# Optimization experiments

Measured on AMD Instinct MI355X. Metric: run time of the kernel, lower is better.

## Reference

```python
import jax, jax.numpy as jnp
import numpy as np

B, S, D = 4, 2048, 1024
E, TOP_K = 8, 2
N_FF = 4096
H = int(2 * N_FF / 3)  # 2730, Expert hidden when ffn_multiplier is None


def setup_inputs() -> dict:
    key = jax.random.key(0)
    ks = jax.random.split(key, 8)
    s = 0.02
    return {
        "x": jax.random.normal(ks[0], (B, S, D), jnp.float32),
        "noise": jax.random.normal(ks[1], (B, S, E), jnp.float32),
        "w_route": jax.random.normal(ks[2], (D, E), jnp.float32) * s,
        "b_route": jnp.zeros((E,), jnp.float32),
        "w_noise": jax.random.normal(ks[3], (D, E), jnp.float32) * s,
        "b_noise": jnp.zeros((E,), jnp.float32),
        "w_proj": jax.random.normal(ks[4], (E, D, 2 * H), jnp.float32) * s,  # SwiGLU proj per expert
        "w_down": jax.random.normal(ks[5], (E, H, D), jnp.float32) * s,
    }


def reference(x, noise, w_route, b_route, w_noise, b_noise, w_proj, w_down):
    b, s, d = x.shape
    e = w_route.shape[1]
    n = b * s
    capacity = int(n * TOP_K / e * 1.0)  # capacity_factor = 1.0

    # --- NoisyTopkRouter (temperature = 1.0) ---
    logits = jnp.einsum("bsd,de->bse", x, w_route) + b_route
    noise_scale = jax.nn.softplus(jnp.einsum("bsd,de->bse", x, w_noise) + b_noise)
    noisy = logits + noise * noise_scale
    top_v, top_i = jax.lax.top_k(noisy, TOP_K)  # [b,s,k]
    # softmax over -inf-filled sparse logits == softmax over the top-k values,
    # scattered back to the expert axis
    probs_k = jax.nn.softmax(top_v, axis=-1)  # [b,s,k]
    routing = jnp.sum(jax.nn.one_hot(top_i, e, dtype=x.dtype) * probs_k[..., None], axis=-2)  # [b,s,e]
    router_prob = routing.mean(axis=(0, 1))
    aux_loss = jnp.sum((router_prob - 1.0 / e) ** 2)

    # --- dispatch ---
    flat_x = x.reshape(n, d)
    flat_gate = routing.reshape(n, e)
    hit = jnp.any(top_i.reshape(n, TOP_K)[:, :, None] == jnp.arange(e)[None, None, :], axis=1)  # [n,e]

    def per_expert(mask_e, gate_e, wp, wd):
        # keep first `capacity` selected tokens, in token order (matches torch nonzero order)
        keep = mask_e & (jnp.cumsum(mask_e) <= capacity)
        sel = jnp.argsort(~keep, stable=True)[:capacity]  # selected token ids first, in order
        valid = keep[sel].astype(flat_x.dtype)
        xin = flat_x[sel]  # [capacity, d]
        x1, x2 = jnp.split(xin @ wp, 2, axis=-1)
        out = (jax.nn.silu(x1) * x2) @ wd  # [capacity, d]
        w = gate_e[sel] * valid
        return sel, out * w[:, None]

    sel, contrib = jax.vmap(per_expert)(hit.T, flat_gate.T, w_proj, w_down)  # [e,cap], [e,cap,d]
    updates = jnp.zeros_like(flat_x).at[sel.reshape(-1)].add(contrib.reshape(-1, d))
    return updates.reshape(b, s, d), aux_loss
```

## Files before the change

kernel.cpp:

```cpp
#include <hip/hip_runtime.h>
#include <cstdint>
#include <cstddef>

#define NTOK 8192
#define DMODEL 1024
#define NEXP 8
#define CAP 2048
#define HFF 2730
#define HFF2 5460
#define KPAD 2752

typedef float f32x4 __attribute__((ext_vector_type(4)));
typedef __attribute__((ext_vector_type(8))) short short8;

__device__ inline unsigned short f2bf(float f) {
  union { float f; unsigned u; } v; v.f = f;
  unsigned u = v.u;
  return (unsigned short)((u + 0x7FFFu + ((u >> 16) & 1u)) >> 16);
}
__device__ inline float bf2f(unsigned short s) {
  union { unsigned u; float f; } v; v.u = ((unsigned)s) << 16; return v.f;
}

typedef __attribute__((address_space(1))) const void g_void;
typedef __attribute__((address_space(3))) void l_void;
__device__ __forceinline__ void dma16(const void* g, void* l) {
  __builtin_amdgcn_global_load_lds((g_void*)g, (l_void*)l, 16, 0, 0);
}
__device__ __forceinline__ void keep(short8 v) { asm volatile("" :: "v"(v)); }

__global__ void cast_x_kernel(const float* __restrict__ x, unsigned short* __restrict__ xb) {
  size_t i = ((size_t)blockIdx.x * 256 + threadIdx.x) * 8;
  float4 v0 = *(const float4*)(x + i);
  float4 v1 = *(const float4*)(x + i + 4);
  union { short8 v; unsigned short s[8]; } p;
  p.s[0] = f2bf(v0.x); p.s[1] = f2bf(v0.y); p.s[2] = f2bf(v0.z); p.s[3] = f2bf(v0.w);
  p.s[4] = f2bf(v1.x); p.s[5] = f2bf(v1.y); p.s[6] = f2bf(v1.z); p.s[7] = f2bf(v1.w);
  *(short8*)(xb + i) = p.v;
}

__global__ void router_kernel(const float* __restrict__ x,
                              const float* __restrict__ noise,
                              const float* __restrict__ w_route,
                              const float* __restrict__ b_route,
                              const float* __restrict__ w_noise,
                              const float* __restrict__ b_noise,
                              int* __restrict__ topi,
                              float* __restrict__ gates) {
  const int lane = threadIdx.x & 63;
  const int wave = threadIdx.x >> 6;
  const int tok = blockIdx.x * 4 + wave;
  const float* xr = x + (size_t)tok * DMODEL;

  double aR[8], aN[8];
#pragma unroll
  for (int e = 0; e < 8; e++) { aR[e] = 0.0; aN[e] = 0.0; }

  for (int d = lane; d < DMODEL; d += 64) {
    double xv = (double)xr[d];
    const float* wr = w_route + d * 8;
    const float* wn = w_noise + d * 8;
#pragma unroll
    for (int e = 0; e < 8; e++) {
      aR[e] += xv * (double)wr[e];
      aN[e] += xv * (double)wn[e];
    }
  }
#pragma unroll
  for (int off = 32; off > 0; off >>= 1) {
#pragma unroll
    for (int e = 0; e < 8; e++) {
      aR[e] += __shfl_down(aR[e], (unsigned)off, 64);
      aN[e] += __shfl_down(aN[e], (unsigned)off, 64);
    }
  }
  if (lane == 0) {
    double nv[8];
#pragma unroll
    for (int e = 0; e < 8; e++) {
      double lg = aR[e] + (double)b_route[e];
      double ns = aN[e] + (double)b_noise[e];
      double sp = fmax(ns, 0.0) + log1p(exp(-fabs(ns)));
      nv[e] = lg + (double)noise[(size_t)tok * 8 + e] * sp;
    }
    int i0 = 0;
#pragma unroll
    for (int e = 1; e < 8; e++) if (nv[e] > nv[i0]) i0 = e;
    int i1 = (i0 == 0) ? 1 : 0;
#pragma unroll
    for (int e = 0; e < 8; e++) if (e != i0 && nv[e] > nv[i1]) i1 = e;
    double r = exp(nv[i1] - nv[i0]);
    float g0 = (float)(1.0 / (1.0 + r));
    float g1 = (float)(r / (1.0 + r));
    topi[tok * 2] = i0; topi[tok * 2 + 1] = i1;
    gates[tok * 2] = g0; gates[tok * 2 + 1] = g1;
  }
}

__global__ void aux_kernel(const int* __restrict__ topi,
                           const float* __restrict__ gates,
                           float* __restrict__ out) {
  const int t = threadIdx.x;
  float s[8];
#pragma unroll
  for (int e = 0; e < 8; e++) s[e] = 0.f;
  for (int i = t; i < NTOK; i += 256) {
    int i0 = topi[2 * i], i1 = topi[2 * i + 1];
    float g0 = gates[2 * i], g1 = gates[2 * i + 1];
#pragma unroll
    for (int e = 0; e < 8; e++)
      s[e] += (i0 == e ? g0 : 0.f) + (i1 == e ? g1 : 0.f);
  }
  __shared__ float sh[256][8];
#pragma unroll
  for (int e = 0; e < 8; e++) sh[t][e] = s[e];
  __syncthreads();
  for (int stride = 128; stride > 0; stride >>= 1) {
    if (t < stride) {
#pragma unroll
      for (int e = 0; e < 8; e++) sh[t][e] += sh[t + stride][e];
    }
    __syncthreads();
  }
  if (t == 0) {
    float aux = 0.f;
#pragma unroll
    for (int e = 0; e < 8; e++) {
      float p = sh[0][e] / (float)NTOK - 0.125f;
      aux += p * p;
    }
    out[(size_t)NTOK * DMODEL] = aux;
  }
}

__global__ void dispatch_kernel(const int* __restrict__ topi,
                                const float* __restrict__ gates,
                                int* __restrict__ sel,
                                float* __restrict__ gsel,
                                int* __restrict__ slot) {
  const int e = blockIdx.x;
  const int t = threadIdx.x;
  const int lane = t & 63;
  const int w = t >> 6;
  __shared__ int waveCnt[16];
  __shared__ int runningS;
  if (t == 0) runningS = 0;
  __syncthreads();

  for (int base = 0; base < NTOK; base += 1024) {
    int tok = base + t;
    int i0 = topi[2 * tok], i1 = topi[2 * tok + 1];
    bool hit = (i0 == e) || (i1 == e);
    int kth = (i0 == e) ? 0 : 1;
    float g = gates[2 * tok + kth];
    unsigned long long m = __ballot(hit);
    int prefix = __popcll(m & ((1ull << lane) - 1ull));
    if (lane == 63) waveCnt[w] = prefix + (hit ? 1 : 0);
    __syncthreads();
    int off = runningS;
    for (int ww = 0; ww < w; ww++) off += waveCnt[ww];
    int pos = off + prefix;
    if (hit) {
      if (pos < CAP) {
        sel[e * CAP + pos] = tok; gsel[e * CAP + pos] = g;
        slot[2 * tok + kth] = pos;
      } else {
        slot[2 * tok + kth] = -1;
      }
    }
    __syncthreads();
    if (t == 0) {
      int sacc = 0;
#pragma unroll
      for (int ww = 0; ww < 16; ww++) sacc += waveCnt[ww];
      runningS += sacc;
    }
    __syncthreads();
  }
  for (int p = runningS + t; p < CAP; p += 1024) { sel[e * CAP + p] = 0; gsel[e * CAP + p] = 0.f; }
}

__global__ void transpose_wp_kernel(const float* __restrict__ wp,
                                    unsigned short* __restrict__ wpT) {
  const int e = blockIdx.z, d0 = blockIdx.y * 32, f0 = blockIdx.x * 32;
  __shared__ unsigned short tile[32][33];
  const int t = threadIdx.x;
  {
    int ld = t >> 3, lf4 = (t & 7) * 4;
    if (f0 + lf4 < HFF2) {
      float4 v = *(const float4*)(wp + (size_t)e * DMODEL * HFF2 + (size_t)(d0 + ld) * HFF2 + f0 + lf4);
      tile[ld][lf4 + 0] = f2bf(v.x);
      tile[ld][lf4 + 1] = f2bf(v.y);
      tile[ld][lf4 + 2] = f2bf(v.z);
      tile[ld][lf4 + 3] = f2bf(v.w);
    }
  }
  __syncthreads();
  {
    int lf = t >> 3, ldq = (t & 7) * 4;
    if (f0 + lf < HFF2) {
      ushort4 o = make_ushort4(tile[ldq + 0][lf], tile[ldq + 1][lf],
                               tile[ldq + 2][lf], tile[ldq + 3][lf]);
      *(ushort4*)(wpT + (size_t)e * HFF2 * DMODEL + (size_t)(f0 + lf) * DMODEL + d0 + ldq) = o;
    }
  }
}

__global__ void transpose_wd_kernel(const float* __restrict__ wd,
                                    unsigned short* __restrict__ wdT) {
  const int e = blockIdx.z, d0 = blockIdx.y * 32, k0 = blockIdx.x * 32;
  __shared__ unsigned short tile[32][33];
  const int t = threadIdx.x;
  {
    int lk = t >> 3, ld4 = (t & 7) * 4;
    int k = k0 + lk;
    if (k < HFF) {
      float4 v = *(const float4*)(wd + (size_t)e * HFF * DMODEL + (size_t)k * DMODEL + d0 + ld4);
      tile[lk][ld4 + 0] = f2bf(v.x);
      tile[lk][ld4 + 1] = f2bf(v.y);
      tile[lk][ld4 + 2] = f2bf(v.z);
      tile[lk][ld4 + 3] = f2bf(v.w);
    } else {
      tile[lk][ld4 + 0] = 0; tile[lk][ld4 + 1] = 0;
      tile[lk][ld4 + 2] = 0; tile[lk][ld4 + 3] = 0;
    }
  }
  __syncthreads();
  {
    int ld = t >> 3, lkq = (t & 7) * 4;
    ushort4 o = make_ushort4(tile[lkq + 0][ld], tile[lkq + 1][ld],
                             tile[lkq + 2][ld], tile[lkq + 3][ld]);
    *(ushort4*)(wdT + (size_t)e * DMODEL * KPAD + (size_t)(d0 + ld) * KPAD + k0 + lkq) = o;
  }
}

__global__ __launch_bounds__(512, 2)
void gemm1_kernel(const unsigned short* __restrict__ xb,
                  const unsigned short* __restrict__ wpT,
                  const int* __restrict__ sel,
                  unsigned short* __restrict__ h) {
  const int e = blockIdx.z;
  const int m0 = blockIdx.x * 256;
  const int n0 = blockIdx.y * 128;

  __shared__ __align__(16) unsigned short smem[4 * 16384];

  const int t = threadIdx.x;
  const int lane = t & 63;
  const int w = t >> 6;
  const int wr = w >> 2;
  const int wc = w & 3;
  const int fr = lane & 15;
  const int fq = lane >> 4;
  const int csw = (fq ^ ((fr >> 1) & 3)) * 8;

  const int r0 = t >> 2;
  const int sw = ((t & 3) ^ ((t >> 3) & 3)) * 8;
  const int tok0 = sel[e * CAP + m0 + r0];
  const int tok1 = sel[e * CAP + m0 + 128 + r0];
  const unsigned short* ga0 = xb + (size_t)tok0 * DMODEL + sw;
  const unsigned short* ga1 = xb + (size_t)tok1 * DMODEL + sw;
  const size_t ebase = (size_t)e * HFF2;
  int c0 = n0 + r0; if (c0 >= HFF) c0 = HFF - 1;
  const unsigned short* gb1 = wpT + (ebase + (size_t)c0) * DMODEL + sw;
  const unsigned short* gb2 = wpT + (ebase + (size_t)(HFF + c0)) * DMODEL + sw;

  const int dOff = w * 1024;

  f32x4 acc1[8][2], acc2[8][2];
#pragma unroll
  for (int i = 0; i < 8; i++)
#pragma unroll
    for (int j = 0; j < 2; j++) { acc1[i][j] = (f32x4)0.f; acc2[i][j] = (f32x4)0.f; }

  auto stageA = [&](int kt) {
    char* b = (char*)smem + (size_t)(kt & 3) * 32768;
    const int k0 = kt * 32;
    dma16(ga0 + k0, b + dOff);
    dma16(ga1 + k0, b + 8192 + dOff);
  };
  auto stageB = [&](int kt) {
    char* b = (char*)smem + (size_t)(kt & 3) * 32768;
    const int k0 = kt * 32;
    dma16(gb1 + k0, b + 16384 + dOff);
    dma16(gb2 + k0, b + 24576 + dOff);
  };

  stageA(0); stageB(0); stageA(1); stageB(1); stageA(2); stageB(2);

  for (int kt = 0; kt < 32; ++kt) {
    if (kt < 30)       asm volatile("s_waitcnt vmcnt(8)" ::: "memory");
    else if (kt == 30) asm volatile("s_waitcnt vmcnt(4)" ::: "memory");
    else               asm volatile("s_waitcnt vmcnt(0)" ::: "memory");
    __builtin_amdgcn_s_barrier();
    asm volatile("" ::: "memory");

    const unsigned short* Ab  = smem + (kt & 3) * 16384;
    const unsigned short* B1b = Ab + 8192;
    const unsigned short* B2b = Ab + 12288;

    short8 a[4], b1[2], b2[2];
#pragma unroll
    for (int i = 0; i < 4; i++) {
      a[i] = *(const short8*)(Ab + (wr * 128 + i * 16 + fr) * 32 + csw);
      keep(a[i]);
    }
#pragma unroll
    for (int j = 0; j < 2; j++) {
      b1[j] = *(const short8*)(B1b + (wc * 32 + j * 16 + fr) * 32 + csw);
      b2[j] = *(const short8*)(B2b + (wc * 32 + j * 16 + fr) * 32 + csw);
      keep(b1[j]); keep(b2[j]);
    }
    if (kt < 29) stageA(kt + 3);
    __builtin_amdgcn_s_barrier();
    asm volatile("s_waitcnt lgkmcnt(0)" ::: "memory");
    __builtin_amdgcn_sched_barrier(0);
    __builtin_amdgcn_s_setprio(1);
#pragma unroll
    for (int i = 0; i < 4; i++)
#pragma unroll
      for (int j = 0; j < 2; j++) {
        acc1[i][j] = __builtin_amdgcn_mfma_f32_16x16x32_bf16(a[i], b1[j], acc1[i][j], 0, 0, 0);
        acc2[i][j] = __builtin_amdgcn_mfma_f32_16x16x32_bf16(a[i], b2[j], acc2[i][j], 0, 0, 0);
      }
    __builtin_amdgcn_s_setprio(0);
    __builtin_amdgcn_sched_barrier(0);
    __builtin_amdgcn_s_barrier();

    short8 a2[4];
#pragma unroll
    for (int i = 0; i < 4; i++) {
      a2[i] = *(const short8*)(Ab + (wr * 128 + (i + 4) * 16 + fr) * 32 + csw);
      keep(a2[i]);
    }
    if (kt < 29) stageB(kt + 3);
    __builtin_amdgcn_s_barrier();
    asm volatile("s_waitcnt lgkmcnt(0)" ::: "memory");
    __builtin_amdgcn_sched_barrier(0);
    __builtin_amdgcn_s_setprio(1);
#pragma unroll
    for (int i = 0; i < 4; i++)
#pragma unroll
      for (int j = 0; j < 2; j++) {
        acc1[i + 4][j] = __builtin_amdgcn_mfma_f32_16x16x32_bf16(a2[i], b1[j], acc1[i + 4][j], 0, 0, 0);
        acc2[i + 4][j] = __builtin_amdgcn_mfma_f32_16x16x32_bf16(a2[i], b2[j], acc2[i + 4][j], 0, 0, 0);
      }
    __builtin_amdgcn_s_setprio(0);
    __builtin_amdgcn_sched_barrier(0);
  }

#pragma unroll
  for (int i = 0; i < 8; i++) {
#pragma unroll
    for (int j = 0; j < 2; j++) {
      const int col = n0 + wc * 32 + j * 16 + fr;
      if (col < KPAD) {
#pragma unroll
        for (int r = 0; r < 4; r++) {
          const int row = m0 + wr * 128 + i * 16 + fq * 4 + r;
          float v1 = acc1[i][j][r], v2 = acc2[i][j][r];
          float hv = (col < HFF) ? (v1 / (1.f + __expf(-v1))) * v2 : 0.f;
          h[((size_t)e * CAP + row) * KPAD + col] = f2bf(hv);
        }
      }
    }
  }
}

__global__ __launch_bounds__(512, 2)
void gemm2_kernel(const unsigned short* __restrict__ h,
                  const unsigned short* __restrict__ wdT,
                  unsigned short* __restrict__ contrib) {
  const int e = blockIdx.z;
  const int m0 = blockIdx.x * 256;
  const int n0 = blockIdx.y * 256;

  __shared__ __align__(16) unsigned short smem[4 * 16384];

  const int t = threadIdx.x;
  const int lane = t & 63;
  const int w = t >> 6;
  const int wr = w >> 2;
  const int wc = w & 3;
  const int fr = lane & 15;
  const int fq = lane >> 4;
  const int csw = (fq ^ ((fr >> 1) & 3)) * 8;

  const int r0 = t >> 2;
  const int sw = ((t & 3) ^ ((t >> 3) & 3)) * 8;
  const unsigned short* ga0 = h + ((size_t)e * CAP + m0 + r0) * KPAD + sw;
  const unsigned short* ga1 = h + ((size_t)e * CAP + m0 + 128 + r0) * KPAD + sw;
  const unsigned short* gb0 = wdT + ((size_t)e * DMODEL + n0 + r0) * KPAD + sw;
  const unsigned short* gb1 = wdT + ((size_t)e * DMODEL + n0 + 128 + r0) * KPAD + sw;

  const int dOff = w * 1024;

  f32x4 acc[8][4];
#pragma unroll
  for (int i = 0; i < 8; i++)
#pragma unroll
    for (int j = 0; j < 4; j++) acc[i][j] = (f32x4)0.f;

  auto stageA = [&](int kt) {
    char* b = (char*)smem + (size_t)(kt & 3) * 32768;
    const int k0 = kt * 32;
    dma16(ga0 + k0, b + dOff);
    dma16(ga1 + k0, b + 8192 + dOff);
  };
  auto stageB = [&](int kt) {
    char* b = (char*)smem + (size_t)(kt & 3) * 32768;
    const int k0 = kt * 32;
    dma16(gb0 + k0, b + 16384 + dOff);
    dma16(gb1 + k0, b + 24576 + dOff);
  };

  stageA(0); stageB(0); stageA(1); stageB(1); stageA(2); stageB(2);

  for (int kt = 0; kt < 86; ++kt) {
    if (kt < 84)       asm volatile("s_waitcnt vmcnt(8)" ::: "memory");
    else if (kt == 84) asm volatile("s_waitcnt vmcnt(4)" ::: "memory");
    else               asm volatile("s_waitcnt vmcnt(0)" ::: "memory");
    __builtin_amdgcn_s_barrier();
    asm volatile("" ::: "memory");

    const unsigned short* Ab = smem + (kt & 3) * 16384;
    const unsigned short* Bb = Ab + 8192;

    short8 a[4], b[4];
#pragma unroll
    for (int i = 0; i < 4; i++) {
      a[i] = *(const short8*)(Ab + (wr * 128 + i * 16 + fr) * 32 + csw);
      keep(a[i]);
    }
#pragma unroll
    for (int j = 0; j < 4; j++) {
      b[j] = *(const short8*)(Bb + (wc * 64 + j * 16 + fr) * 32 + csw);
      keep(b[j]);
    }
    if (kt < 83) stageA(kt + 3);
    __builtin_amdgcn_s_barrier();
    asm volatile("s_waitcnt lgkmcnt(0)" ::: "memory");
    __builtin_amdgcn_sched_barrier(0);
    __builtin_amdgcn_s_setprio(1);
#pragma unroll
    for (int i = 0; i < 4; i++)
#pragma unroll
      for (int j = 0; j < 4; j++)
        acc[i][j] = __builtin_amdgcn_mfma_f32_16x16x32_bf16(a[i], b[j], acc[i][j], 0, 0, 0);
    __builtin_amdgcn_s_setprio(0);
    __builtin_amdgcn_sched_barrier(0);
    __builtin_amdgcn_s_barrier();

    short8 a2[4];
#pragma unroll
    for (int i = 0; i < 4; i++) {
      a2[i] = *(const short8*)(Ab + (wr * 128 + (i + 4) * 16 + fr) * 32 + csw);
      keep(a2[i]);
    }
    if (kt < 83) stageB(kt + 3);
    __builtin_amdgcn_s_barrier();
    asm volatile("s_waitcnt lgkmcnt(0)" ::: "memory");
    __builtin_amdgcn_sched_barrier(0);
    __builtin_amdgcn_s_setprio(1);
#pragma unroll
    for (int i = 0; i < 4; i++)
#pragma unroll
      for (int j = 0; j < 4; j++)
        acc[i + 4][j] = __builtin_amdgcn_mfma_f32_16x16x32_bf16(a2[i], b[j], acc[i + 4][j], 0, 0, 0);
    __builtin_amdgcn_s_setprio(0);
    __builtin_amdgcn_sched_barrier(0);
  }

#pragma unroll
  for (int i = 0; i < 8; i++) {
#pragma unroll
    for (int j = 0; j < 4; j++) {
      const int col = n0 + wc * 64 + j * 16 + fr;
#pragma unroll
      for (int r = 0; r < 4; r++) {
        const int row = m0 + wr * 128 + i * 16 + fq * 4 + r;
        contrib[((size_t)e * CAP + row) * DMODEL + col] = f2bf(acc[i][j][r]);
      }
    }
  }
}

__global__ void combine_kernel(const unsigned short* __restrict__ contrib,
                               const int* __restrict__ topi,
                               const int* __restrict__ slot,
                               const float* __restrict__ gates,
                               float* __restrict__ out) {
  const int tok = blockIdx.x;
  const int t = threadIdx.x;
  const int e0 = topi[2 * tok], e1 = topi[2 * tok + 1];
  const int s0 = slot[2 * tok], s1 = slot[2 * tok + 1];
  const float g0 = gates[2 * tok], g1 = gates[2 * tok + 1];
  float4 acc = make_float4(0.f, 0.f, 0.f, 0.f);
  if (s0 >= 0) {
    ushort4 c = *(const ushort4*)(contrib + ((size_t)(e0 * CAP + s0)) * DMODEL + t * 4);
    acc.x += g0 * bf2f(c.x); acc.y += g0 * bf2f(c.y);
    acc.z += g0 * bf2f(c.z); acc.w += g0 * bf2f(c.w);
  }
  if (s1 >= 0) {
    ushort4 c = *(const ushort4*)(contrib + ((size_t)(e1 * CAP + s1)) * DMODEL + t * 4);
    acc.x += g1 * bf2f(c.x); acc.y += g1 * bf2f(c.y);
    acc.z += g1 * bf2f(c.z); acc.w += g1 * bf2f(c.w);
  }
  *(float4*)(out + (size_t)tok * DMODEL + t * 4) = acc;
}

extern "C" void kernel_launch(void* const* d_in, const int* in_sizes, int n_in,
                              void* d_out, int out_size, void* d_ws, size_t ws_size,
                              hipStream_t stream) {
  const float* x = (const float*)d_in[0];
  const float* noise = (const float*)d_in[1];
  const float* w_route = (const float*)d_in[2];
  const float* b_route = (const float*)d_in[3];
  const float* w_noise = (const float*)d_in[4];
  const float* b_noise = (const float*)d_in[5];
  const float* w_proj = (const float*)d_in[6];
  const float* w_down = (const float*)d_in[7];
  float* out = (float*)d_out;

  char* ws = (char*)d_ws;
  const size_t WT_BYTES = (size_t)NEXP * HFF2 * DMODEL * 2;
  const size_t WDT_BYTES = (size_t)NEXP * DMODEL * KPAD * 2;
  const size_t H_BYTES = (size_t)NEXP * CAP * KPAD * 2;
  unsigned short* wT = (unsigned short*)ws;
  unsigned short* contrib = (unsigned short*)(ws + WDT_BYTES);
  unsigned short* hbuf = (unsigned short*)(ws + WT_BYTES);
  char* p = ws + WT_BYTES + H_BYTES;
  int* sel = (int*)p;          p += (size_t)NEXP * CAP * 4;
  float* gsel = (float*)p;     p += (size_t)NEXP * CAP * 4;
  int* topi = (int*)p;         p += (size_t)NTOK * 2 * 4;
  float* gates = (float*)p;    p += (size_t)NTOK * 2 * 4;
  int* slot = (int*)p;

  unsigned short* xb = (unsigned short*)d_out;

  hipLaunchKernelGGL(cast_x_kernel, dim3(NTOK * DMODEL / (256 * 8)), dim3(256), 0, stream, x, xb);
  hipLaunchKernelGGL(router_kernel, dim3(NTOK / 4), dim3(256), 0, stream,
                     x, noise, w_route, b_route, w_noise, b_noise, topi, gates);
  hipLaunchKernelGGL(dispatch_kernel, dim3(NEXP), dim3(1024), 0, stream, topi, gates, sel, gsel, slot);
  hipLaunchKernelGGL(transpose_wp_kernel, dim3(171, 32, NEXP), dim3(256), 0, stream, w_proj, wT);
  hipLaunchKernelGGL(gemm1_kernel, dim3(CAP / 256, 22, NEXP), dim3(512), 0, stream, xb, wT, sel, hbuf);
  hipLaunchKernelGGL(transpose_wd_kernel, dim3(KPAD / 32, DMODEL / 32, NEXP), dim3(256), 0, stream, w_down, wT);
  hipLaunchKernelGGL(gemm2_kernel, dim3(CAP / 256, DMODEL / 256, NEXP), dim3(512), 0, stream,
                     hbuf, wT, contrib);
  hipLaunchKernelGGL(combine_kernel, dim3(NTOK), dim3(256), 0, stream,
                     contrib, topi, slot, gates, out);
  hipLaunchKernelGGL(aux_kernel, dim3(1), dim3(256), 0, stream, topi, gates, out);
}
```

Baseline: 836.4 us.

## Widen wp transpose tiles to 64x64 and drop scheduling fences in GEMM loops

The w_proj transpose now uses 64x64 tiles with four float4 loads per thread and writes 16-byte rows of bf16, storing into shared memory already transposed. This cuts block count and uses wider global stores to speed up the fp32-to-bf16 weight transpose. Separately, both GEMM main loops drop the asm keep() register pins and the sched_barrier fences, leaving the compiler free to interleave LDS reads with MFMAs. That can improve overlap, but it risks the compiler reordering loads past the hand-placed barriers and waitcnts.

```diff
diff --git a/kernel.cpp b/kernel.cpp
--- a/kernel.cpp
+++ b/kernel.cpp
@@ -27,7 +27,6 @@
 __device__ __forceinline__ void dma16(const void* g, void* l) {
   __builtin_amdgcn_global_load_lds((g_void*)g, (l_void*)l, 16, 0, 0);
 }
-__device__ __forceinline__ void keep(short8 v) { asm volatile("" :: "v"(v)); }
 
 __global__ void cast_x_kernel(const float* __restrict__ x, unsigned short* __restrict__ xb) {
   size_t i = ((size_t)blockIdx.x * 256 + threadIdx.x) * 8;
@@ -182,26 +181,35 @@
 
 __global__ void transpose_wp_kernel(const float* __restrict__ wp,
                                     unsigned short* __restrict__ wpT) {
-  const int e = blockIdx.z, d0 = blockIdx.y * 32, f0 = blockIdx.x * 32;
-  __shared__ unsigned short tile[32][33];
-  const int t = threadIdx.x;
-  {
-    int ld = t >> 3, lf4 = (t & 7) * 4;
-    if (f0 + lf4 < HFF2) {
-      float4 v = *(const float4*)(wp + (size_t)e * DMODEL * HFF2 + (size_t)(d0 + ld) * HFF2 + f0 + lf4);
-      tile[ld][lf4 + 0] = f2bf(v.x);
-      tile[ld][lf4 + 1] = f2bf(v.y);
-      tile[ld][lf4 + 2] = f2bf(v.z);
-      tile[ld][lf4 + 3] = f2bf(v.w);
+  const int e = blockIdx.z, d0 = blockIdx.y * 64, f0 = blockIdx.x * 64;
+  __shared__ unsigned short tile[64][68];
+  const int t = threadIdx.x;
+  const int ld = t >> 4;
+  const int lf4 = (t & 15) * 4;
+#pragma unroll
+  for (int p = 0; p < 4; p++) {
+    int d = d0 + p * 16 + ld;
+    int f = f0 + lf4;
+    if (f < HFF2) {
+      float4 v = *(const float4*)(wp + ((size_t)e * DMODEL + d) * HFF2 + f);
+      tile[lf4 + 0][p * 16 + ld] = f2bf(v.x);
+      tile[lf4 + 1][p * 16 + ld] = f2bf(v.y);
+      tile[lf4 + 2][p * 16 + ld] = f2bf(v.z);
+      tile[lf4 + 3][p * 16 + ld] = f2bf(v.w);
     }
   }
   __syncthreads();
-  {
-    int lf = t >> 3, ldq = (t & 7) * 4;
-    if (f0 + lf < HFF2) {
-      ushort4 o = make_ushort4(tile[ldq + 0][lf], tile[ldq + 1][lf],
-                               tile[ldq + 2][lf], tile[ldq + 3][lf]);
-      *(ushort4*)(wpT + (size_t)e * HFF2 * DMODEL + (size_t)(f0 + lf) * DMODEL + d0 + ldq) = o;
+  const int dq = (t & 7) * 8;
+#pragma unroll
+  for (int q = 0; q < 2; q++) {
+    int fl = q * 32 + (t >> 3);
+    int f = f0 + fl;
+    if (f < HFF2) {
+      ushort4 u0 = *(const ushort4*)&tile[fl][dq];
+      ushort4 u1 = *(const ushort4*)&tile[fl][dq + 4];
+      union { ushort4 u[2]; short8 v; } pk;
+      pk.u[0] = u0; pk.u[1] = u1;
+      *(short8*)(wpT + (size_t)e * HFF2 * DMODEL + (size_t)f * DMODEL + d0 + dq) = pk.v;
     }
   }
 }
@@ -301,20 +309,16 @@
 
     short8 a[4], b1[2], b2[2];
 #pragma unroll
-    for (int i = 0; i < 4; i++) {
+    for (int i = 0; i < 4; i++)
       a[i] = *(const short8*)(Ab + (wr * 128 + i * 16 + fr) * 32 + csw);
-      keep(a[i]);
-    }
 #pragma unroll
     for (int j = 0; j < 2; j++) {
       b1[j] = *(const short8*)(B1b + (wc * 32 + j * 16 + fr) * 32 + csw);
       b2[j] = *(const short8*)(B2b + (wc * 32 + j * 16 + fr) * 32 + csw);
-      keep(b1[j]); keep(b2[j]);
     }
     if (kt < 29) stageA(kt + 3);
     __builtin_amdgcn_s_barrier();
     asm volatile("s_waitcnt lgkmcnt(0)" ::: "memory");
-    __builtin_amdgcn_sched_barrier(0);
     __builtin_amdgcn_s_setprio(1);
 #pragma unroll
     for (int i = 0; i < 4; i++)
@@ -324,19 +328,15 @@
         acc2[i][j] = __builtin_amdgcn_mfma_f32_16x16x32_bf16(a[i], b2[j], acc2[i][j], 0, 0, 0);
       }
     __builtin_amdgcn_s_setprio(0);
-    __builtin_amdgcn_sched_barrier(0);
     __builtin_amdgcn_s_barrier();
 
     short8 a2[4];
 #pragma unroll
-    for (int i = 0; i < 4; i++) {
+    for (int i = 0; i < 4; i++)
       a2[i] = *(const short8*)(Ab + (wr * 128 + (i + 4) * 16 + fr) * 32 + csw);
-      keep(a2[i]);
-    }
     if (kt < 29) stageB(kt + 3);
     __builtin_amdgcn_s_barrier();
     asm volatile("s_waitcnt lgkmcnt(0)" ::: "memory");
-    __builtin_amdgcn_sched_barrier(0);
     __builtin_amdgcn_s_setprio(1);
 #pragma unroll
     for (int i = 0; i < 4; i++)
@@ -346,7 +346,6 @@
         acc2[i + 4][j] = __builtin_amdgcn_mfma_f32_16x16x32_bf16(a2[i], b2[j], acc2[i + 4][j], 0, 0, 0);
       }
     __builtin_amdgcn_s_setprio(0);
-    __builtin_amdgcn_sched_barrier(0);
   }
 
 #pragma unroll
@@ -428,19 +427,14 @@
 
     short8 a[4], b[4];
 #pragma unroll
-    for (int i = 0; i < 4; i++) {
+    for (int i = 0; i < 4; i++)
       a[i] = *(const short8*)(Ab + (wr * 128 + i * 16 + fr) * 32 + csw);
-      keep(a[i]);
-    }
-#pragma unroll
-    for (int j = 0; j < 4; j++) {
+#pragma unroll
+    for (int j = 0; j < 4; j++)
       b[j] = *(const short8*)(Bb + (wc * 64 + j * 16 + fr) * 32 + csw);
-      keep(b[j]);
-    }
     if (kt < 83) stageA(kt + 3);
     __builtin_amdgcn_s_barrier();
     asm volatile("s_waitcnt lgkmcnt(0)" ::: "memory");
-    __builtin_amdgcn_sched_barrier(0);
     __builtin_amdgcn_s_setprio(1);
 #pragma unroll
     for (int i = 0; i < 4; i++)
@@ -448,19 +442,15 @@
       for (int j = 0; j < 4; j++)
         acc[i][j] = __builtin_amdgcn_mfma_f32_16x16x32_bf16(a[i], b[j], acc[i][j], 0, 0, 0);
     __builtin_amdgcn_s_setprio(0);
-    __builtin_amdgcn_sched_barrier(0);
     __builtin_amdgcn_s_barrier();
 
     short8 a2[4];
 #pragma unroll
-    for (int i = 0; i < 4; i++) {
+    for (int i = 0; i < 4; i++)
       a2[i] = *(const short8*)(Ab + (wr * 128 + (i + 4) * 16 + fr) * 32 + csw);
-      keep(a2[i]);
-    }
     if (kt < 83) stageB(kt + 3);
     __builtin_amdgcn_s_barrier();
     asm volatile("s_waitcnt lgkmcnt(0)" ::: "memory");
-    __builtin_amdgcn_sched_barrier(0);
     __builtin_amdgcn_s_setprio(1);
 #pragma unroll
     for (int i = 0; i < 4; i++)
@@ -468,7 +458,6 @@
       for (int j = 0; j < 4; j++)
         acc[i + 4][j] = __builtin_amdgcn_mfma_f32_16x16x32_bf16(a2[i], b[j], acc[i + 4][j], 0, 0, 0);
     __builtin_amdgcn_s_setprio(0);
-    __builtin_amdgcn_sched_barrier(0);
   }
 
 #pragma unroll
@@ -542,7 +531,7 @@
   hipLaunchKernelGGL(router_kernel, dim3(NTOK / 4), dim3(256), 0, stream,
                      x, noise, w_route, b_route, w_noise, b_noise, topi, gates);
   hipLaunchKernelGGL(dispatch_kernel, dim3(NEXP), dim3(1024), 0, stream, topi, gates, sel, gsel, slot);
-  hipLaunchKernelGGL(transpose_wp_kernel, dim3(171, 32, NEXP), dim3(256), 0, stream, w_proj, wT);
+  hipLaunchKernelGGL(transpose_wp_kernel, dim3(86, 16, NEXP), dim3(256), 0, stream, w_proj, wT);
   hipLaunchKernelGGL(gemm1_kernel, dim3(CAP / 256, 22, NEXP), dim3(512), 0, stream, xb, wT, sel, hbuf);
   hipLaunchKernelGGL(transpose_wd_kernel, dim3(KPAD / 32, DMODEL / 32, NEXP), dim3(256), 0, stream, w_down, wT);
   hipLaunchKernelGGL(gemm2_kernel, dim3(CAP / 256, DMODEL / 256, NEXP), dim3(512), 0, stream,
```

After: 811.2 us. 1.03x faster.
